# Performance work log

Hardware: AMD Instinct MI355X
Metric: run time of the kernel (lower is better)

## Reference

```python
import jax, jax.numpy as jnp
import numpy as np

N_ITER = 10
TOL = 1e-05
EPS_R = 1e-10
REG = 1e-06
F32_EPS = float(np.finfo(np.float32).eps)


def setup_inputs() -> dict:
    key = jax.random.key(0)
    K, T, F, _ = 6, 2048, 513, 2
    X = jax.random.normal(key, (K, T, F, 2), dtype=jnp.float32)
    return {"X": X}


def _aux_iva_iss(X):
    # X: (K, T, F, 2) real/imag -> complex (F, K, T)
    Xc = (X[..., 0] + 1j * X[..., 1]).astype(jnp.complex64)
    Xc = jnp.transpose(Xc, (2, 0, 1))  # (F, K, T)
    F, K, T = Xc.shape
    eyeK = jnp.eye(K, dtype=jnp.complex64)
    W = jnp.broadcast_to(eyeK, (F, K, K)).astype(jnp.complex64)  # (F, K, K)
    Xh = jnp.conj(Xc)
    done = jnp.array(False)

    for _ in range(N_ITER):
        W_old = W
        # demix: Y[f] = W[f] @ X[f]
        Y = jnp.einsum('fkm,fmt->fkt', W, Xc)
        # per-(source, frame) norms across frequency
        r = jnp.sqrt(jnp.clip(jnp.sum(jnp.abs(Y) ** 2, axis=0), EPS_R))  # (K, T)
        wt = 1.0 / jnp.clip(r, EPS_R)  # laplace contrast g'(r)/r
        # weighted covariances V[f,k] = (X_f * wt[k]) X_f^H / T + reg*I  -> (F, K, K, K)
        V = jnp.einsum('fat,kt,fbt->fkab', Xc, wt.astype(jnp.complex64), Xh) / T
        V = V + REG * eyeK
        # sequential ISS updates over target row k (vectorized over f, m)
        for k in range(K):
            wk = W[:, k, :]  # (F, K)
            wk_c = jnp.conj(wk)
            quad = jnp.einsum('fa,fmab,fb->fm', wk, V, wk_c)  # w_k V_m w_k^H
            denom = jnp.clip(quad.real, EPS_R)  # (F, K)
            num = jnp.einsum('fma,fmab,fb->fm', W, V, wk_c)  # w_m V_m w_k^H
            vk = num / denom  # (F, K)
            vk = vk.at[:, k].set((1.0 - 1.0 / jnp.sqrt(denom[:, k])).astype(jnp.complex64))
            W = W - vk[:, :, None] * wk[:, None, :]
        # emulate early-break on relative change (freeze W once converged)
        W = jnp.where(done, W_old, W)
        diff = jnp.linalg.norm((W - W_old).reshape(-1))
        rel = diff / jnp.clip(jnp.linalg.norm(W_old.reshape(-1)), F32_EPS)
        done = jnp.logical_or(done, rel < TOL)

    Y = jnp.einsum('fkm,fmt->fkt', W, Xc)  # (F, K, T)
    # ref_mic == 0 -> no projection-back rescaling
    Y_out = jnp.transpose(Y, (1, 2, 0))  # (K, T, F)
    return jnp.stack([Y_out.real, Y_out.imag], axis=-1)  # (K, T, F, 2)


def reference(X):
    return _aux_iva_iss(X)
```

## Files before the change

kernel.cpp:

```cpp
#include <hip/hip_runtime.h>
#include <math.h>

#define T_DIM 2048
#define F_DIM 513
#define K_DIM 6
#define N_ITER 10

#define OFF_W    0
#define OFF_WT   36936
#define OFF_V    49224
#define OFF_DONE 270840
#define OFF_PART 270844

__global__ void initW(float* __restrict__ ws) {
    int idx = blockIdx.x * 256 + threadIdx.x;
    if (idx < F_DIM * 36) {
        int e = idx % 36;
        int a = e / 6, b = e % 6;
        ws[OFF_W + idx * 2]     = (a == b) ? 1.0f : 0.0f;
        ws[OFF_W + idx * 2 + 1] = 0.0f;
    }
    if (idx == 0) {
        *(int*)(ws + OFF_DONE) = 0;
    }
}

__global__ __launch_bounds__(256) void transp(const float2* __restrict__ X,
                                              float2* __restrict__ Xt) {
    __shared__ float2 tile[32][33];
    int k  = blockIdx.z;
    int t0 = blockIdx.x * 32;
    int f0 = blockIdx.y * 32;
    int tx = threadIdx.x & 31, ty = threadIdx.x >> 5;
#pragma unroll
    for (int j = 0; j < 4; ++j) {
        int t = t0 + ty + j * 8;
        int f = f0 + tx;
        if (f < F_DIM) tile[ty + j * 8][tx] = X[(k * T_DIM + t) * F_DIM + f];
    }
    __syncthreads();
#pragma unroll
    for (int j = 0; j < 4; ++j) {
        int f = f0 + ty + j * 8;
        int t = t0 + tx;
        if (f < F_DIM) Xt[(f * K_DIM + k) * T_DIM + t] = tile[tx][ty + j * 8];
    }
}

__global__ __launch_bounds__(512) void passA(const float2* __restrict__ X,
                                             float* __restrict__ ws) {
    if (*(const int*)(ws + OFF_DONE)) return;
    const float2* W = (const float2*)(ws + OFF_W);
    float* wt = ws + OFF_WT;
    int t0  = blockIdx.x * 8;
    int tid = threadIdx.x;

    float s[48];
#pragma unroll
    for (int i = 0; i < 48; ++i) s[i] = 0.0f;

    for (int f = tid; f < F_DIM; f += 512) {
        float2 w[36];
#pragma unroll
        for (int i = 0; i < 36; ++i) w[i] = W[f * 36 + i];
#pragma unroll
        for (int tl = 0; tl < 8; ++tl) {
            int t = t0 + tl;
            float2 x[6];
#pragma unroll
            for (int m = 0; m < 6; ++m) x[m] = X[(m * T_DIM + t) * F_DIM + f];
#pragma unroll
            for (int k = 0; k < 6; ++k) {
                float yr = 0.0f, yi = 0.0f;
#pragma unroll
                for (int m = 0; m < 6; ++m) {
                    float2 wk = w[k * 6 + m];
                    yr += wk.x * x[m].x - wk.y * x[m].y;
                    yi += wk.x * x[m].y + wk.y * x[m].x;
                }
                s[k * 8 + tl] += yr * yr + yi * yi;
            }
        }
    }
#pragma unroll
    for (int i = 0; i < 48; ++i) {
        float v = s[i];
#pragma unroll
        for (int d = 1; d < 64; d <<= 1) v += __shfl_xor(v, d);
        s[i] = v;
    }
    __shared__ float part[8][48];
    int wave = tid >> 6, lane = tid & 63;
    if (lane == 0) {
#pragma unroll
        for (int i = 0; i < 48; ++i) part[wave][i] = s[i];
    }
    __syncthreads();
    if (tid < 48) {
        float r2 = 0.0f;
#pragma unroll
        for (int w = 0; w < 8; ++w) r2 += part[w][tid];
        int k = tid >> 3, tl = tid & 7;
        float r = sqrtf(fmaxf(r2, 1e-10f));
        wt[k * T_DIM + t0 + tl] = 1.0f / fmaxf(r, 1e-10f);
    }
}

__global__ __launch_bounds__(64) void passB(const float2* __restrict__ Xt,
                                            float* __restrict__ ws) {
    if (*(const int*)(ws + OFF_DONE)) return;
    const float* wt = ws + OFF_WT;
    float* V = ws + OFF_V;
    int f = blockIdx.x;
    int kg = blockIdx.y;
    int lane = threadIdx.x;

    float accd[3][6];
    float accr[3][15];
    float acci[3][15];
#pragma unroll
    for (int j = 0; j < 3; ++j) {
#pragma unroll
        for (int a = 0; a < 6; ++a) accd[j][a] = 0.0f;
#pragma unroll
        for (int p = 0; p < 15; ++p) { accr[j][p] = 0.0f; acci[j][p] = 0.0f; }
    }

    const float2* xb = Xt + f * K_DIM * T_DIM;
    for (int t = lane; t < T_DIM; t += 64) {
        float w0 = wt[(3 * kg + 0) * T_DIM + t];
        float w1 = wt[(3 * kg + 1) * T_DIM + t];
        float w2 = wt[(3 * kg + 2) * T_DIM + t];
        float2 x[6];
#pragma unroll
        for (int m = 0; m < 6; ++m) x[m] = xb[m * T_DIM + t];
        float od[6], opr[15], opi[15];
#pragma unroll
        for (int a = 0; a < 6; ++a) od[a] = x[a].x * x[a].x + x[a].y * x[a].y;
#pragma unroll
        for (int a = 1; a < 6; ++a) {
#pragma unroll
            for (int b = 0; b < 6; ++b) {
                if (b < a) {
                    int p = a * (a - 1) / 2 + b;
                    opr[p] = x[a].x * x[b].x + x[a].y * x[b].y;
                    opi[p] = x[a].y * x[b].x - x[a].x * x[b].y;
                }
            }
        }
#pragma unroll
        for (int a = 0; a < 6; ++a) {
            accd[0][a] += w0 * od[a];
            accd[1][a] += w1 * od[a];
            accd[2][a] += w2 * od[a];
        }
#pragma unroll
        for (int p = 0; p < 15; ++p) {
            accr[0][p] += w0 * opr[p];  acci[0][p] += w0 * opi[p];
            accr[1][p] += w1 * opr[p];  acci[1][p] += w1 * opi[p];
            accr[2][p] += w2 * opr[p];  acci[2][p] += w2 * opi[p];
        }
    }

    __shared__ float red[108 * 65];
#pragma unroll
    for (int j = 0; j < 3; ++j) {
#pragma unroll
        for (int a = 0; a < 6; ++a) red[(j * 36 + a) * 65 + lane] = accd[j][a];
#pragma unroll
        for (int p = 0; p < 15; ++p) {
            red[(j * 36 + 6 + p) * 65 + lane]  = accr[j][p];
            red[(j * 36 + 21 + p) * 65 + lane] = acci[j][p];
        }
    }
    __syncthreads();
    for (int v = lane; v < 108; v += 64) {
        float sum = 0.0f;
        for (int i = 0; i < 64; ++i) sum += red[v * 65 + i];
        int j = v / 36, e = v % 36;
        int k = 3 * kg + j;
        float* Vf = V + (size_t)((f * K_DIM + k) * 36) * 2;
        float val = sum * (1.0f / (float)T_DIM);
        if (e < 6) {
            Vf[(e * 6 + e) * 2]     = val + 1e-6f;
            Vf[(e * 6 + e) * 2 + 1] = 0.0f;
        } else if (e < 21) {
            int p = e - 6;
            int a = (p < 1) ? 1 : (p < 3) ? 2 : (p < 6) ? 3 : (p < 10) ? 4 : 5;
            int b = p - a * (a - 1) / 2;
            Vf[(a * 6 + b) * 2] = val;
            Vf[(b * 6 + a) * 2] = val;
        } else {
            int p = e - 21;
            int a = (p < 1) ? 1 : (p < 3) ? 2 : (p < 6) ? 3 : (p < 10) ? 4 : 5;
            int b = p - a * (a - 1) / 2;
            Vf[(a * 6 + b) * 2 + 1] =  val;
            Vf[(b * 6 + a) * 2 + 1] = -val;
        }
    }
}

__global__ __launch_bounds__(128) void passC(float* __restrict__ ws) {
    if (*(const int*)(ws + OFF_DONE)) return;
    float* Wg = ws + OFF_W;
    const float* V = ws + OFF_V;
    int tid = threadIdx.x;
    int fl = tid >> 3, m = tid & 7;
    int f = blockIdx.x * 16 + fl;
    bool active = (f < F_DIM) && (m < 6);

    __shared__ float Wl[16][6][6][2];
    float v[36][2];
    float w[6][2], wold[6][2];

    if (active) {
        const float* Vp = V + (size_t)((f * K_DIM + m) * 36) * 2;
#pragma unroll
        for (int i = 0; i < 36; ++i) { v[i][0] = Vp[2 * i]; v[i][1] = Vp[2 * i + 1]; }
        const float* Wp = Wg + (f * 36 + m * 6) * 2;
#pragma unroll
        for (int a = 0; a < 6; ++a) {
            w[a][0] = Wp[2 * a]; w[a][1] = Wp[2 * a + 1];
            wold[a][0] = w[a][0]; wold[a][1] = w[a][1];
            Wl[fl][m][a][0] = w[a][0]; Wl[fl][m][a][1] = w[a][1];
        }
    }
    __syncthreads();

    for (int k = 0; k < 6; ++k) {
        float wk[6][2];
        if (active) {
#pragma unroll
            for (int a = 0; a < 6; ++a) {
                wk[a][0] = Wl[fl][k][a][0];
                wk[a][1] = Wl[fl][k][a][1];
            }
        }
        __syncthreads();
        if (active) {
            float t[6][2];
#pragma unroll
            for (int a = 0; a < 6; ++a) {
                float tr = 0.0f, ti = 0.0f;
#pragma unroll
                for (int b = 0; b < 6; ++b) {
                    float vr = v[a * 6 + b][0], vi = v[a * 6 + b][1];
                    tr += vr * wk[b][0] + vi * wk[b][1];
                    ti += vi * wk[b][0] - vr * wk[b][1];
                }
                t[a][0] = tr; t[a][1] = ti;
            }
            float quad_r = 0.0f, num_r = 0.0f, num_i = 0.0f;
#pragma unroll
            for (int a = 0; a < 6; ++a) {
                quad_r += wk[a][0] * t[a][0] - wk[a][1] * t[a][1];
                num_r  += w[a][0] * t[a][0] - w[a][1] * t[a][1];
                num_i  += w[a][0] * t[a][1] + w[a][1] * t[a][0];
            }
            float denom = fmaxf(quad_r, 1e-10f);
            float vkr, vki;
            if (m == k) {
                vkr = 1.0f - 1.0f / sqrtf(denom);
                vki = 0.0f;
            } else {
                float inv = 1.0f / denom;
                vkr = num_r * inv;
                vki = num_i * inv;
            }
#pragma unroll
            for (int a = 0; a < 6; ++a) {
                w[a][0] -= vkr * wk[a][0] - vki * wk[a][1];
                w[a][1] -= vkr * wk[a][1] + vki * wk[a][0];
            }
#pragma unroll
            for (int a = 0; a < 6; ++a) {
                Wl[fl][m][a][0] = w[a][0];
                Wl[fl][m][a][1] = w[a][1];
            }
        }
        __syncthreads();
    }

    float d2 = 0.0f, o2 = 0.0f;
    if (active) {
        float* Wp = Wg + (f * 36 + m * 6) * 2;
#pragma unroll
        for (int a = 0; a < 6; ++a) {
            Wp[2 * a] = w[a][0]; Wp[2 * a + 1] = w[a][1];
            float dr = w[a][0] - wold[a][0], di = w[a][1] - wold[a][1];
            d2 += dr * dr + di * di;
            o2 += wold[a][0] * wold[a][0] + wold[a][1] * wold[a][1];
        }
    }
#pragma unroll
    for (int d = 1; d < 64; d <<= 1) {
        d2 += __shfl_xor(d2, d);
        o2 += __shfl_xor(o2, d);
    }
    __shared__ float rb[4];
    if ((tid & 63) == 0) { rb[(tid >> 6) * 2] = d2; rb[(tid >> 6) * 2 + 1] = o2; }
    __syncthreads();
    if (tid == 0) {
        ws[OFF_PART + 2 * blockIdx.x]     = rb[0] + rb[2];
        ws[OFF_PART + 2 * blockIdx.x + 1] = rb[1] + rb[3];
    }
}

__global__ void convk(float* __restrict__ ws) {
    if (threadIdx.x != 0) return;
    int* done = (int*)(ws + OFF_DONE);
    if (*done) return;
    float d2 = 0.0f, o2 = 0.0f;
    for (int b = 0; b < 33; ++b) {
        d2 += ws[OFF_PART + 2 * b];
        o2 += ws[OFF_PART + 2 * b + 1];
    }
    float rel = sqrtf(d2) / fmaxf(sqrtf(o2), 1.1920929e-07f);
    if (rel < 1e-5f) *done = 1;
}

__global__ __launch_bounds__(512) void finalY(const float2* __restrict__ X,
                                              const float* __restrict__ ws,
                                              float2* __restrict__ out) {
    const float2* W = (const float2*)(ws + OFF_W);
    int t = blockIdx.x;
    for (int f = threadIdx.x; f < F_DIM; f += 512) {
        float2 w[36];
#pragma unroll
        for (int i = 0; i < 36; ++i) w[i] = W[f * 36 + i];
        float2 x[6];
#pragma unroll
        for (int m = 0; m < 6; ++m) x[m] = X[(m * T_DIM + t) * F_DIM + f];
#pragma unroll
        for (int k = 0; k < 6; ++k) {
            float yr = 0.0f, yi = 0.0f;
#pragma unroll
            for (int m = 0; m < 6; ++m) {
                float2 wk = w[k * 6 + m];
                yr += wk.x * x[m].x - wk.y * x[m].y;
                yi += wk.x * x[m].y + wk.y * x[m].x;
            }
            out[(k * T_DIM + t) * F_DIM + f] = make_float2(yr, yi);
        }
    }
}

extern "C" void kernel_launch(void* const* d_in, const int* in_sizes, int n_in,
                              void* d_out, int out_size, void* d_ws, size_t ws_size,
                              hipStream_t stream) {
    const float2* X = (const float2*)d_in[0];
    float* ws = (float*)d_ws;
    float2* out = (float2*)d_out;
    float2* Xt = out;

    initW<<<73, 256, 0, stream>>>(ws);
    transp<<<dim3(64, 17, 6), 256, 0, stream>>>(X, Xt);

    for (int it = 0; it < N_ITER; ++it) {
        passA<<<T_DIM / 8, 512, 0, stream>>>(X, ws);
        passB<<<dim3(F_DIM, 2), 64, 0, stream>>>(Xt, ws);
        passC<<<33, 128, 0, stream>>>(ws);
        convk<<<1, 64, 0, stream>>>(ws);
    }
    finalY<<<T_DIM, 512, 0, stream>>>(X, ws, out);
}
```

Before: 656.3 us.

## Fuse covariance and ISS update per frequency, drop convergence kernel, retile final demix

Merges the covariance build and ISS update into one kernel per frequency, keeping V in shared memory instead of global. The separate convergence kernel is removed: each kernel recomputes the relative-change test redundantly from double-buffered per-frequency partials. W initialisation is folded into the transpose kernel, and finalY is retiled so each thread reuses its W across 32 frames. Fewer launches and less global traffic per iteration, at the cost of redundant reductions and only 6 active threads during the ISS phase.

Result: slower. 735.9 us (+12.1%).

```diff
diff --git a/kernel.cpp b/kernel.cpp
--- a/kernel.cpp
+++ b/kernel.cpp
@@ -3,57 +3,74 @@
 
 #define T_DIM 2048
 #define F_DIM 513
-#define K_DIM 6
 #define N_ITER 10
 
 #define OFF_W    0
 #define OFF_WT   36936
-#define OFF_V    49224
-#define OFF_DONE 270840
-#define OFF_PART 270844
-
-__global__ void initW(float* __restrict__ ws) {
-    int idx = blockIdx.x * 256 + threadIdx.x;
-    if (idx < F_DIM * 36) {
-        int e = idx % 36;
-        int a = e / 6, b = e % 6;
-        ws[OFF_W + idx * 2]     = (a == b) ? 1.0f : 0.0f;
-        ws[OFF_W + idx * 2 + 1] = 0.0f;
-    }
-    if (idx == 0) {
-        *(int*)(ws + OFF_DONE) = 0;
-    }
-}
+#define OFF_P0   49224
+#define OFF_P1   50250
 
 __global__ __launch_bounds__(256) void transp(const float2* __restrict__ X,
-                                              float2* __restrict__ Xt) {
+                                              float2* __restrict__ Xt,
+                                              float* __restrict__ ws) {
+    const int fb  = blockIdx.x + 64 * (blockIdx.y + 17 * blockIdx.z);
+    const int tid = threadIdx.x;
+    if (fb < 73) {
+        int idx = fb * 256 + tid;
+        if (idx < F_DIM * 36) {
+            int e = idx % 36;
+            ws[OFF_W + 2 * idx]     = ((e / 6) == (e % 6)) ? 1.0f : 0.0f;
+            ws[OFF_W + 2 * idx + 1] = 0.0f;
+        }
+    } else if (fb < 78) {
+        int idx = (fb - 73) * 256 + tid;
+        if (idx < 2 * F_DIM) { ws[OFF_P0 + idx] = 1.0f; ws[OFF_P1 + idx] = 1.0f; }
+    }
+
     __shared__ float2 tile[32][33];
-    int k  = blockIdx.z;
-    int t0 = blockIdx.x * 32;
-    int f0 = blockIdx.y * 32;
-    int tx = threadIdx.x & 31, ty = threadIdx.x >> 5;
+    const int k  = blockIdx.z;
+    const int t0 = blockIdx.x * 32;
+    const int f0 = blockIdx.y * 32;
+    const int tx = tid & 31, ty = tid >> 5;
 #pragma unroll
     for (int j = 0; j < 4; ++j) {
         int t = t0 + ty + j * 8;
         int f = f0 + tx;
-        if (f < F_DIM) tile[ty + j * 8][tx] = X[(k * T_DIM + t) * F_DIM + f];
+        if (f < F_DIM) tile[ty + j * 8][tx] = X[((size_t)k * T_DIM + t) * F_DIM + f];
     }
     __syncthreads();
 #pragma unroll
     for (int j = 0; j < 4; ++j) {
         int f = f0 + ty + j * 8;
         int t = t0 + tx;
-        if (f < F_DIM) Xt[(f * K_DIM + k) * T_DIM + t] = tile[tx][ty + j * 8];
+        if (f < F_DIM) Xt[((size_t)f * 6 + k) * T_DIM + t] = tile[tx][ty + j * 8];
     }
 }
 
 __global__ __launch_bounds__(512) void passA(const float2* __restrict__ X,
-                                             float* __restrict__ ws) {
-    if (*(const int*)(ws + OFF_DONE)) return;
-    const float2* W = (const float2*)(ws + OFF_W);
+                                             float* __restrict__ ws,
+                                             const float* __restrict__ pin) {
+    __shared__ float sred[384];
+    const int tid = threadIdx.x, wave = tid >> 6, lane = tid & 63;
+
+    {
+        float d2 = 0.f, o2 = 0.f;
+        for (int i = tid; i < F_DIM; i += 512) { d2 += pin[2 * i]; o2 += pin[2 * i + 1]; }
+#pragma unroll
+        for (int d = 1; d < 64; d <<= 1) { d2 += __shfl_xor(d2, d); o2 += __shfl_xor(o2, d); }
+        if (lane == 0) { sred[wave * 2] = d2; sred[wave * 2 + 1] = o2; }
+        __syncthreads();
+        d2 = 0.f; o2 = 0.f;
+#pragma unroll
+        for (int w = 0; w < 8; ++w) { d2 += sred[w * 2]; o2 += sred[w * 2 + 1]; }
+        float rel = sqrtf(d2) / fmaxf(sqrtf(o2), 1.1920929e-07f);
+        __syncthreads();
+        if (rel < 1e-5f) return;
+    }
+
+    const float2* Wc = (const float2*)(ws + OFF_W);
     float* wt = ws + OFF_WT;
-    int t0  = blockIdx.x * 8;
-    int tid = threadIdx.x;
+    const int t0 = blockIdx.x * 8;
 
     float s[48];
 #pragma unroll
@@ -62,16 +79,16 @@
     for (int f = tid; f < F_DIM; f += 512) {
         float2 w[36];
 #pragma unroll
-        for (int i = 0; i < 36; ++i) w[i] = W[f * 36 + i];
+        for (int i = 0; i < 36; ++i) w[i] = Wc[f * 36 + i];
 #pragma unroll
         for (int tl = 0; tl < 8; ++tl) {
             int t = t0 + tl;
             float2 x[6];
 #pragma unroll
-            for (int m = 0; m < 6; ++m) x[m] = X[(m * T_DIM + t) * F_DIM + f];
+            for (int m = 0; m < 6; ++m) x[m] = X[((size_t)m * T_DIM + t) * F_DIM + f];
 #pragma unroll
             for (int k = 0; k < 6; ++k) {
-                float yr = 0.0f, yi = 0.0f;
+                float yr = 0.f, yi = 0.f;
 #pragma unroll
                 for (int m = 0; m < 6; ++m) {
                     float2 wk = w[k * 6 + m];
@@ -89,258 +106,249 @@
         for (int d = 1; d < 64; d <<= 1) v += __shfl_xor(v, d);
         s[i] = v;
     }
-    __shared__ float part[8][48];
-    int wave = tid >> 6, lane = tid & 63;
     if (lane == 0) {
 #pragma unroll
-        for (int i = 0; i < 48; ++i) part[wave][i] = s[i];
+        for (int i = 0; i < 48; ++i) sred[wave * 48 + i] = s[i];
     }
     __syncthreads();
     if (tid < 48) {
-        float r2 = 0.0f;
-#pragma unroll
-        for (int w = 0; w < 8; ++w) r2 += part[w][tid];
+        float r2 = 0.f;
+#pragma unroll
+        for (int w = 0; w < 8; ++w) r2 += sred[w * 48 + tid];
         int k = tid >> 3, tl = tid & 7;
         float r = sqrtf(fmaxf(r2, 1e-10f));
         wt[k * T_DIM + t0 + tl] = 1.0f / fmaxf(r, 1e-10f);
     }
 }
 
-__global__ __launch_bounds__(64) void passB(const float2* __restrict__ Xt,
-                                            float* __restrict__ ws) {
-    if (*(const int*)(ws + OFF_DONE)) return;
-    const float* wt = ws + OFF_WT;
-    float* V = ws + OFF_V;
-    int f = blockIdx.x;
-    int kg = blockIdx.y;
-    int lane = threadIdx.x;
-
-    float accd[3][6];
-    float accr[3][15];
-    float acci[3][15];
+__global__ __launch_bounds__(128) void passBC(const float2* __restrict__ Xt,
+                                              float* __restrict__ ws,
+                                              const float* __restrict__ pin,
+                                              float* __restrict__ pout) {
+    __shared__ float red[2 * 108 * 17];
+    __shared__ float VL[432];
+    __shared__ float WL[72];
+    __shared__ float sc[4];
+    const int bid = blockIdx.x;
+    const int tid = threadIdx.x, wv = tid >> 6, lane = tid & 63;
+
+    {
+        float d2 = 0.f, o2 = 0.f;
+        for (int i = tid; i < F_DIM; i += 128) { d2 += pin[2 * i]; o2 += pin[2 * i + 1]; }
+#pragma unroll
+        for (int d = 1; d < 64; d <<= 1) { d2 += __shfl_xor(d2, d); o2 += __shfl_xor(o2, d); }
+        if (lane == 0) { sc[wv * 2] = d2; sc[wv * 2 + 1] = o2; }
+        __syncthreads();
+        d2 = sc[0] + sc[2]; o2 = sc[1] + sc[3];
+        float rel = sqrtf(d2) / fmaxf(sqrtf(o2), 1.1920929e-07f);
+        __syncthreads();
+        if (rel < 1e-5f) {
+            if (tid == 0) { pout[2 * bid] = 0.0f; pout[2 * bid + 1] = 1.0f; }
+            return;
+        }
+    }
+
+    const int f = bid;
+    float accd[3][6], accr[3][15], acci[3][15];
 #pragma unroll
     for (int j = 0; j < 3; ++j) {
 #pragma unroll
-        for (int a = 0; a < 6; ++a) accd[j][a] = 0.0f;
-#pragma unroll
-        for (int p = 0; p < 15; ++p) { accr[j][p] = 0.0f; acci[j][p] = 0.0f; }
-    }
-
-    const float2* xb = Xt + f * K_DIM * T_DIM;
+        for (int a = 0; a < 6; ++a) accd[j][a] = 0.f;
+#pragma unroll
+        for (int p = 0; p < 15; ++p) { accr[j][p] = 0.f; acci[j][p] = 0.f; }
+    }
+    const float2* xb = Xt + (size_t)f * 6 * T_DIM;
+    const float* wt0 = ws + OFF_WT + (3 * wv) * T_DIM;
     for (int t = lane; t < T_DIM; t += 64) {
-        float w0 = wt[(3 * kg + 0) * T_DIM + t];
-        float w1 = wt[(3 * kg + 1) * T_DIM + t];
-        float w2 = wt[(3 * kg + 2) * T_DIM + t];
+        float g0 = wt0[t], g1 = wt0[T_DIM + t], g2 = wt0[2 * T_DIM + t];
         float2 x[6];
 #pragma unroll
-        for (int m = 0; m < 6; ++m) x[m] = xb[m * T_DIM + t];
-        float od[6], opr[15], opi[15];
+        for (int m = 0; m < 6; ++m) x[m] = xb[(size_t)m * T_DIM + t];
+        float od[6];
 #pragma unroll
         for (int a = 0; a < 6; ++a) od[a] = x[a].x * x[a].x + x[a].y * x[a].y;
-#pragma unroll
-        for (int a = 1; a < 6; ++a) {
-#pragma unroll
-            for (int b = 0; b < 6; ++b) {
-                if (b < a) {
-                    int p = a * (a - 1) / 2 + b;
-                    opr[p] = x[a].x * x[b].x + x[a].y * x[b].y;
-                    opi[p] = x[a].y * x[b].x - x[a].x * x[b].y;
-                }
-            }
-        }
+        float opr[15], opi[15];
+#pragma unroll
+        for (int a = 1; a < 6; ++a)
+#pragma unroll
+            for (int b = 0; b < a; ++b) {
+                const int p = a * (a - 1) / 2 + b;
+                opr[p] = x[a].x * x[b].x + x[a].y * x[b].y;
+                opi[p] = x[a].y * x[b].x - x[a].x * x[b].y;
+            }
 #pragma unroll
         for (int a = 0; a < 6; ++a) {
-            accd[0][a] += w0 * od[a];
-            accd[1][a] += w1 * od[a];
-            accd[2][a] += w2 * od[a];
+            accd[0][a] += g0 * od[a];
+            accd[1][a] += g1 * od[a];
+            accd[2][a] += g2 * od[a];
         }
 #pragma unroll
         for (int p = 0; p < 15; ++p) {
-            accr[0][p] += w0 * opr[p];  acci[0][p] += w0 * opi[p];
-            accr[1][p] += w1 * opr[p];  acci[1][p] += w1 * opi[p];
-            accr[2][p] += w2 * opr[p];  acci[2][p] += w2 * opi[p];
-        }
-    }
-
-    __shared__ float red[108 * 65];
+            accr[0][p] += g0 * opr[p]; acci[0][p] += g0 * opi[p];
+            accr[1][p] += g1 * opr[p]; acci[1][p] += g1 * opi[p];
+            accr[2][p] += g2 * opr[p]; acci[2][p] += g2 * opi[p];
+        }
+    }
 #pragma unroll
     for (int j = 0; j < 3; ++j) {
 #pragma unroll
-        for (int a = 0; a < 6; ++a) red[(j * 36 + a) * 65 + lane] = accd[j][a];
+        for (int a = 0; a < 6; ++a) {
+            float v = accd[j][a];
+            v += __shfl_xor(v, 1); v += __shfl_xor(v, 2);
+            if ((lane & 3) == 0) red[(wv * 108 + j * 36 + a) * 17 + (lane >> 2)] = v;
+        }
 #pragma unroll
         for (int p = 0; p < 15; ++p) {
-            red[(j * 36 + 6 + p) * 65 + lane]  = accr[j][p];
-            red[(j * 36 + 21 + p) * 65 + lane] = acci[j][p];
-        }
-    }
-    __syncthreads();
-    for (int v = lane; v < 108; v += 64) {
-        float sum = 0.0f;
-        for (int i = 0; i < 64; ++i) sum += red[v * 65 + i];
-        int j = v / 36, e = v % 36;
-        int k = 3 * kg + j;
-        float* Vf = V + (size_t)((f * K_DIM + k) * 36) * 2;
-        float val = sum * (1.0f / (float)T_DIM);
+            float vr = accr[j][p];
+            vr += __shfl_xor(vr, 1); vr += __shfl_xor(vr, 2);
+            float vi = acci[j][p];
+            vi += __shfl_xor(vi, 1); vi += __shfl_xor(vi, 2);
+            if ((lane & 3) == 0) {
+                red[(wv * 108 + j * 36 + 6 + p) * 17 + (lane >> 2)]  = vr;
+                red[(wv * 108 + j * 36 + 21 + p) * 17 + (lane >> 2)] = vi;
+            }
+        }
+    }
+    __syncthreads();
+    for (int v = tid; v < 216; v += 128) {
+        float sum = 0.f;
+#pragma unroll
+        for (int i = 0; i < 16; ++i) sum += red[v * 17 + i];
+        sum *= (1.0f / (float)T_DIM);
+        int w = v / 108, rem = v % 108;
+        int j = rem / 36, e = rem % 36;
+        int k = 3 * w + j;
         if (e < 6) {
-            Vf[(e * 6 + e) * 2]     = val + 1e-6f;
-            Vf[(e * 6 + e) * 2 + 1] = 0.0f;
+            VL[((k * 6 + e) * 6 + e) * 2]     = sum + 1e-6f;
+            VL[((k * 6 + e) * 6 + e) * 2 + 1] = 0.f;
         } else if (e < 21) {
             int p = e - 6;
             int a = (p < 1) ? 1 : (p < 3) ? 2 : (p < 6) ? 3 : (p < 10) ? 4 : 5;
             int b = p - a * (a - 1) / 2;
-            Vf[(a * 6 + b) * 2] = val;
-            Vf[(b * 6 + a) * 2] = val;
+            VL[((k * 6 + a) * 6 + b) * 2] = sum;
+            VL[((k * 6 + b) * 6 + a) * 2] = sum;
         } else {
             int p = e - 21;
             int a = (p < 1) ? 1 : (p < 3) ? 2 : (p < 6) ? 3 : (p < 10) ? 4 : 5;
             int b = p - a * (a - 1) / 2;
-            Vf[(a * 6 + b) * 2 + 1] =  val;
-            Vf[(b * 6 + a) * 2 + 1] = -val;
-        }
-    }
-}
-
-__global__ __launch_bounds__(128) void passC(float* __restrict__ ws) {
-    if (*(const int*)(ws + OFF_DONE)) return;
-    float* Wg = ws + OFF_W;
-    const float* V = ws + OFF_V;
-    int tid = threadIdx.x;
-    int fl = tid >> 3, m = tid & 7;
-    int f = blockIdx.x * 16 + fl;
-    bool active = (f < F_DIM) && (m < 6);
-
-    __shared__ float Wl[16][6][6][2];
-    float v[36][2];
-    float w[6][2], wold[6][2];
-
-    if (active) {
-        const float* Vp = V + (size_t)((f * K_DIM + m) * 36) * 2;
-#pragma unroll
-        for (int i = 0; i < 36; ++i) { v[i][0] = Vp[2 * i]; v[i][1] = Vp[2 * i + 1]; }
-        const float* Wp = Wg + (f * 36 + m * 6) * 2;
+            VL[((k * 6 + a) * 6 + b) * 2 + 1] =  sum;
+            VL[((k * 6 + b) * 6 + a) * 2 + 1] = -sum;
+        }
+    }
+    __syncthreads();
+
+    float vm[36][2];
+    float w6[6][2], wold[6][2];
+    const int m = tid;
+    if (tid < 6) {
+#pragma unroll
+        for (int i = 0; i < 36; ++i) {
+            vm[i][0] = VL[(m * 36 + i) * 2];
+            vm[i][1] = VL[(m * 36 + i) * 2 + 1];
+        }
+        float* Wp = ws + OFF_W + ((size_t)f * 36 + m * 6) * 2;
 #pragma unroll
         for (int a = 0; a < 6; ++a) {
-            w[a][0] = Wp[2 * a]; w[a][1] = Wp[2 * a + 1];
-            wold[a][0] = w[a][0]; wold[a][1] = w[a][1];
-            Wl[fl][m][a][0] = w[a][0]; Wl[fl][m][a][1] = w[a][1];
-        }
-    }
-    __syncthreads();
-
+            w6[a][0] = Wp[2 * a]; w6[a][1] = Wp[2 * a + 1];
+            wold[a][0] = w6[a][0]; wold[a][1] = w6[a][1];
+            WL[(m * 6 + a) * 2] = w6[a][0]; WL[(m * 6 + a) * 2 + 1] = w6[a][1];
+        }
+    }
+    __syncthreads();
     for (int k = 0; k < 6; ++k) {
         float wk[6][2];
-        if (active) {
-#pragma unroll
-            for (int a = 0; a < 6; ++a) {
-                wk[a][0] = Wl[fl][k][a][0];
-                wk[a][1] = Wl[fl][k][a][1];
-            }
-        }
-        __syncthreads();
-        if (active) {
-            float t[6][2];
-#pragma unroll
-            for (int a = 0; a < 6; ++a) {
-                float tr = 0.0f, ti = 0.0f;
+        if (tid < 6) {
+#pragma unroll
+            for (int a = 0; a < 6; ++a) {
+                wk[a][0] = WL[(k * 6 + a) * 2];
+                wk[a][1] = WL[(k * 6 + a) * 2 + 1];
+            }
+        }
+        __syncthreads();
+        if (tid < 6) {
+            float t6[6][2];
+#pragma unroll
+            for (int a = 0; a < 6; ++a) {
+                float tr = 0.f, ti = 0.f;
 #pragma unroll
                 for (int b = 0; b < 6; ++b) {
-                    float vr = v[a * 6 + b][0], vi = v[a * 6 + b][1];
+                    float vr = vm[a * 6 + b][0], vi = vm[a * 6 + b][1];
                     tr += vr * wk[b][0] + vi * wk[b][1];
                     ti += vi * wk[b][0] - vr * wk[b][1];
                 }
-                t[a][0] = tr; t[a][1] = ti;
-            }
-            float quad_r = 0.0f, num_r = 0.0f, num_i = 0.0f;
-#pragma unroll
-            for (int a = 0; a < 6; ++a) {
-                quad_r += wk[a][0] * t[a][0] - wk[a][1] * t[a][1];
-                num_r  += w[a][0] * t[a][0] - w[a][1] * t[a][1];
-                num_i  += w[a][0] * t[a][1] + w[a][1] * t[a][0];
-            }
-            float denom = fmaxf(quad_r, 1e-10f);
+                t6[a][0] = tr; t6[a][1] = ti;
+            }
+            float quad = 0.f, nr = 0.f, ni = 0.f;
+#pragma unroll
+            for (int a = 0; a < 6; ++a) {
+                quad += wk[a][0] * t6[a][0] - wk[a][1] * t6[a][1];
+                nr   += w6[a][0] * t6[a][0] - w6[a][1] * t6[a][1];
+                ni   += w6[a][0] * t6[a][1] + w6[a][1] * t6[a][0];
+            }
+            float denom = fmaxf(quad, 1e-10f);
             float vkr, vki;
-            if (m == k) {
-                vkr = 1.0f - 1.0f / sqrtf(denom);
-                vki = 0.0f;
-            } else {
-                float inv = 1.0f / denom;
-                vkr = num_r * inv;
-                vki = num_i * inv;
-            }
-#pragma unroll
-            for (int a = 0; a < 6; ++a) {
-                w[a][0] -= vkr * wk[a][0] - vki * wk[a][1];
-                w[a][1] -= vkr * wk[a][1] + vki * wk[a][0];
-            }
-#pragma unroll
-            for (int a = 0; a < 6; ++a) {
-                Wl[fl][m][a][0] = w[a][0];
-                Wl[fl][m][a][1] = w[a][1];
-            }
-        }
-        __syncthreads();
-    }
-
-    float d2 = 0.0f, o2 = 0.0f;
-    if (active) {
-        float* Wp = Wg + (f * 36 + m * 6) * 2;
+            if (m == k) { vkr = 1.0f - 1.0f / sqrtf(denom); vki = 0.0f; }
+            else { float inv = 1.0f / denom; vkr = nr * inv; vki = ni * inv; }
+#pragma unroll
+            for (int a = 0; a < 6; ++a) {
+                w6[a][0] -= vkr * wk[a][0] - vki * wk[a][1];
+                w6[a][1] -= vkr * wk[a][1] + vki * wk[a][0];
+            }
+#pragma unroll
+            for (int a = 0; a < 6; ++a) {
+                WL[(m * 6 + a) * 2]     = w6[a][0];
+                WL[(m * 6 + a) * 2 + 1] = w6[a][1];
+            }
+        }
+        __syncthreads();
+    }
+    float d2 = 0.f, o2 = 0.f;
+    if (tid < 6) {
+        float* Wp = ws + OFF_W + ((size_t)f * 36 + m * 6) * 2;
 #pragma unroll
         for (int a = 0; a < 6; ++a) {
-            Wp[2 * a] = w[a][0]; Wp[2 * a + 1] = w[a][1];
-            float dr = w[a][0] - wold[a][0], di = w[a][1] - wold[a][1];
+            Wp[2 * a] = w6[a][0]; Wp[2 * a + 1] = w6[a][1];
+            float dr = w6[a][0] - wold[a][0], di = w6[a][1] - wold[a][1];
             d2 += dr * dr + di * di;
             o2 += wold[a][0] * wold[a][0] + wold[a][1] * wold[a][1];
         }
     }
 #pragma unroll
-    for (int d = 1; d < 64; d <<= 1) {
+    for (int d = 1; d < 8; d <<= 1) {
         d2 += __shfl_xor(d2, d);
         o2 += __shfl_xor(o2, d);
     }
-    __shared__ float rb[4];
-    if ((tid & 63) == 0) { rb[(tid >> 6) * 2] = d2; rb[(tid >> 6) * 2 + 1] = o2; }
-    __syncthreads();
     if (tid == 0) {
-        ws[OFF_PART + 2 * blockIdx.x]     = rb[0] + rb[2];
-        ws[OFF_PART + 2 * blockIdx.x + 1] = rb[1] + rb[3];
-    }
-}
-
-__global__ void convk(float* __restrict__ ws) {
-    if (threadIdx.x != 0) return;
-    int* done = (int*)(ws + OFF_DONE);
-    if (*done) return;
-    float d2 = 0.0f, o2 = 0.0f;
-    for (int b = 0; b < 33; ++b) {
-        d2 += ws[OFF_PART + 2 * b];
-        o2 += ws[OFF_PART + 2 * b + 1];
-    }
-    float rel = sqrtf(d2) / fmaxf(sqrtf(o2), 1.1920929e-07f);
-    if (rel < 1e-5f) *done = 1;
-}
-
-__global__ __launch_bounds__(512) void finalY(const float2* __restrict__ X,
+        pout[2 * bid]     = d2;
+        pout[2 * bid + 1] = o2;
+    }
+}
+
+__global__ __launch_bounds__(256) void finalY(const float2* __restrict__ X,
                                               const float* __restrict__ ws,
                                               float2* __restrict__ out) {
-    const float2* W = (const float2*)(ws + OFF_W);
-    int t = blockIdx.x;
-    for (int f = threadIdx.x; f < F_DIM; f += 512) {
-        float2 w[36];
-#pragma unroll
-        for (int i = 0; i < 36; ++i) w[i] = W[f * 36 + i];
+    const int f  = blockIdx.y * 256 + threadIdx.x;
+    const int t0 = blockIdx.x * 32;
+    if (f >= F_DIM) return;
+    const float2* Wf = (const float2*)(ws + OFF_W) + (size_t)f * 36;
+    float2 w[36];
+#pragma unroll
+    for (int i = 0; i < 36; ++i) w[i] = Wf[i];
+    for (int tl = 0; tl < 32; ++tl) {
+        int t = t0 + tl;
         float2 x[6];
 #pragma unroll
-        for (int m = 0; m < 6; ++m) x[m] = X[(m * T_DIM + t) * F_DIM + f];
+        for (int m = 0; m < 6; ++m) x[m] = X[((size_t)m * T_DIM + t) * F_DIM + f];
 #pragma unroll
         for (int k = 0; k < 6; ++k) {
-            float yr = 0.0f, yi = 0.0f;
+            float yr = 0.f, yi = 0.f;
 #pragma unroll
             for (int m = 0; m < 6; ++m) {
                 float2 wk = w[k * 6 + m];
                 yr += wk.x * x[m].x - wk.y * x[m].y;
                 yi += wk.x * x[m].y + wk.y * x[m].x;
             }
-            out[(k * T_DIM + t) * F_DIM + f] = make_float2(yr, yi);
+            out[((size_t)k * T_DIM + t) * F_DIM + f] = make_float2(yr, yi);
         }
     }
 }
@@ -348,19 +356,18 @@
 extern "C" void kernel_launch(void* const* d_in, const int* in_sizes, int n_in,
                               void* d_out, int out_size, void* d_ws, size_t ws_size,
                               hipStream_t stream) {
+    (void)in_sizes; (void)n_in; (void)out_size; (void)ws_size;
     const float2* X = (const float2*)d_in[0];
     float* ws = (float*)d_ws;
     float2* out = (float2*)d_out;
     float2* Xt = out;
 
-    initW<<<73, 256, 0, stream>>>(ws);
-    transp<<<dim3(64, 17, 6), 256, 0, stream>>>(X, Xt);
-
+    transp<<<dim3(64, 17, 6), 256, 0, stream>>>(X, Xt, ws);
     for (int it = 0; it < N_ITER; ++it) {
-        passA<<<T_DIM / 8, 512, 0, stream>>>(X, ws);
-        passB<<<dim3(F_DIM, 2), 64, 0, stream>>>(Xt, ws);
-        passC<<<33, 128, 0, stream>>>(ws);
-        convk<<<1, 64, 0, stream>>>(ws);
-    }
-    finalY<<<T_DIM, 512, 0, stream>>>(X, ws, out);
-}
+        const float* pin = ws + (((it + 1) & 1) ? OFF_P1 : OFF_P0);
+        float* pout      = ws + (((it    ) & 1) ? OFF_P1 : OFF_P0);
+        passA<<<T_DIM / 8, 512, 0, stream>>>(X, ws, pin);
+        passBC<<<F_DIM, 128, 0, stream>>>(Xt, ws, pin, pout);
+    }
+    finalY<<<dim3(T_DIM / 32, 3), 256, 0, stream>>>(X, ws, out);
+}
```
